# Performance work log

Hardware: AMD Instinct MI355X
Metric: run time of the kernel (lower is better)

## Reference

```python
import jax, jax.numpy as jnp
import numpy as np

B, S, H = 2, 2048, 4096
NH, NKV, HD = 32, 8, 128
N_REP = NH // NKV
SCALING = HD ** -0.5


def rotate_half(x):
    x1, x2 = x[..., : HD // 2], x[..., HD // 2 :]
    return jnp.concatenate((-x2, x1), axis=-1)


def setup_inputs() -> dict:
    key = jax.random.key(0)
    ks = jax.random.split(key, 8)
    hidden_states = jax.random.normal(ks[0], (B, S, H), dtype=jnp.float32)
    # RoPE tables computed as in Llama (deterministic, realistic values)
    inv_freq = 1.0 / (10000.0 ** (jnp.arange(0, HD, 2, dtype=jnp.float32) / HD))
    t = jnp.arange(S, dtype=jnp.float32)
    freqs = jnp.einsum('s,d->sd', t, inv_freq)
    emb = jnp.concatenate((freqs, freqs), axis=-1)  # [S, HD]
    cos = jnp.broadcast_to(jnp.cos(emb)[None], (B, S, HD))
    sin = jnp.broadcast_to(jnp.sin(emb)[None], (B, S, HD))
    # additive causal mask [B,1,S,S]
    causal = jnp.where(jnp.tril(jnp.ones((S, S), dtype=bool)), 0.0, -1e9).astype(jnp.float32)
    attention_mask = jnp.broadcast_to(causal[None, None], (B, 1, S, S))
    std = 0.02
    Wq = jax.random.normal(ks[1], (NH * HD, H), dtype=jnp.float32) * std
    Wk = jax.random.normal(ks[2], (NKV * HD, H), dtype=jnp.float32) * std
    Wv = jax.random.normal(ks[3], (NKV * HD, H), dtype=jnp.float32) * std
    Wo = jax.random.normal(ks[4], (H, NH * HD), dtype=jnp.float32) * std
    return dict(hidden_states=hidden_states, cos=cos, sin=sin,
                attention_mask=attention_mask, Wq=Wq, Wk=Wk, Wv=Wv, Wo=Wo)


def reference(hidden_states, cos, sin, attention_mask, Wq, Wk, Wv, Wo):
    b, s, _ = hidden_states.shape
    # projections (torch Linear: x @ W.T), split into heads -> [B, nH, S, HD]
    q = (hidden_states @ Wq.T).reshape(b, s, NH, HD).transpose(0, 2, 1, 3)
    k = (hidden_states @ Wk.T).reshape(b, s, NKV, HD).transpose(0, 2, 1, 3)
    v = (hidden_states @ Wv.T).reshape(b, s, NKV, HD).transpose(0, 2, 1, 3)
    # RoPE: cos/sin [B,S,HD] -> [B,1,S,HD]
    c, sn = cos[:, None], sin[:, None]
    q = q * c + rotate_half(q) * sn
    k = k * c + rotate_half(k) * sn
    # GQA: repeat kv heads
    k = jnp.repeat(k, N_REP, axis=1)
    v = jnp.repeat(v, N_REP, axis=1)
    scores = jnp.einsum('bhqd,bhkd->bhqk', q, k) * SCALING + attention_mask
    attn = jax.nn.softmax(scores.astype(jnp.float32), axis=-1).astype(q.dtype)
    out = jnp.einsum('bhqk,bhkd->bhqd', attn, v)
    out = out.transpose(0, 2, 1, 3).reshape(b, s, NH * HD)
    return out @ Wo.T
```

## Files before the change

kernel.cpp:

```cpp
#include <hip/hip_runtime.h>
#include <stdint.h>

typedef unsigned short u16;
typedef __attribute__((ext_vector_type(8))) short short8;
typedef __attribute__((ext_vector_type(4))) float f32x4;
typedef __attribute__((ext_vector_type(16))) float f32x16;
typedef __attribute__((ext_vector_type(4))) u16 u16x4;

static constexpr float SCALE = 0.08838834764831845f;
static constexpr float QSCALE = 0.12752459769642898f;

__device__ __forceinline__ u16 f2bf(float f) {
    union { float f; unsigned u; } x; x.f = f;
    unsigned r = x.u + 0x7fffu + ((x.u >> 16) & 1u);
    return (u16)(r >> 16);
}
__device__ __forceinline__ float bf2f(u16 b) {
    union { unsigned u; float f; } x; x.u = ((unsigned)b) << 16;
    return x.f;
}
__device__ __forceinline__ unsigned cvt_pk_bf16(float lo, float hi_) {
    unsigned r;
    asm("v_cvt_pk_bf16_f32 %0, %1, %2" : "=v"(r) : "v"(lo), "v"(hi_));
    return r;
}

__global__ __launch_bounds__(256) void convert5_kernel(const float* __restrict__ s0, const float* __restrict__ s1,
                                                       const float* __restrict__ s2, const float* __restrict__ s3,
                                                       const float* __restrict__ s4,
                                                       u16* __restrict__ d0, u16* __restrict__ d1,
                                                       u16* __restrict__ d2, u16* __restrict__ d3,
                                                       u16* __restrict__ d4) {
    const int V0 = 4194304, V1 = 8388608, V2 = 9437184, V3 = 10485760, V4 = 14680064;
    const int stride = gridDim.x * blockDim.x;
    for (int i = blockIdx.x * blockDim.x + threadIdx.x; i < V4; i += stride) {
        const float* sp; u16* dp; int off;
        if (i < V0)      { sp = s0; dp = d0; off = i; }
        else if (i < V1) { sp = s1; dp = d1; off = i - V0; }
        else if (i < V2) { sp = s2; dp = d2; off = i - V1; }
        else if (i < V3) { sp = s3; dp = d3; off = i - V2; }
        else             { sp = s4; dp = d4; off = i - V3; }
        float4 v = *reinterpret_cast<const float4*>(sp + (size_t)off * 4);
        u16x4 o;
        o.x = f2bf(v.x); o.y = f2bf(v.y); o.z = f2bf(v.z); o.w = f2bf(v.w);
        *reinterpret_cast<u16x4*>(dp + (size_t)off * 4) = o;
    }
}

template<int OUT_MODE>
__global__ __launch_bounds__(256) void gemm_bt(const u16* __restrict__ A,
                                               const u16* __restrict__ B,
                                               void* __restrict__ Cv,
                                               int M, int N, int K) {
    constexpr int BK = 64;
    __shared__ u16 sA[128 * BK];
    __shared__ u16 sB[128 * BK];
    const int tid = threadIdx.x;
    const int wid = tid >> 6, lane = tid & 63;
    const int lrow = lane & 15, lgrp = lane >> 4;
    const int row0 = blockIdx.x * 128, col0 = blockIdx.y * 128;
    const int wr = (wid >> 1) * 64, wc = (wid & 1) * 64;

    f32x4 acc[4][4] = {};

    const int NT = K / BK;
    for (int kt = 0; kt < NT; ++kt) {
        const int k0 = kt * BK;
        __syncthreads();
        #pragma unroll
        for (int rnd = 0; rnd < 4; ++rnd) {
            const int eoff = (rnd * 256 + tid) * 8;
            const int r = eoff >> 6, c = eoff & 63;
            const int gc = c ^ ((r & 7) << 3);
            const int ldsoff = rnd * 2048 + wid * 512;
            __builtin_amdgcn_global_load_lds(
                (const __attribute__((address_space(1))) void*)(A + (size_t)(row0 + r) * K + k0 + gc),
                (__attribute__((address_space(3))) void*)(&sA[ldsoff]), 16, 0, 0);
            __builtin_amdgcn_global_load_lds(
                (const __attribute__((address_space(1))) void*)(B + (size_t)(col0 + r) * K + k0 + gc),
                (__attribute__((address_space(3))) void*)(&sB[ldsoff]), 16, 0, 0);
        }
        __syncthreads();
        #pragma unroll
        for (int kk = 0; kk < 2; ++kk) {
            const int koff = kk * 32 + lgrp * 8;
            short8 af[4], bfr[4];
            #pragma unroll
            for (int m = 0; m < 4; ++m) {
                const int rr = wr + m * 16 + lrow;
                af[m] = *(const short8*)&sA[rr * BK + (koff ^ ((rr & 7) << 3))];
            }
            #pragma unroll
            for (int n = 0; n < 4; ++n) {
                const int rr = wc + n * 16 + lrow;
                bfr[n] = *(const short8*)&sB[rr * BK + (koff ^ ((rr & 7) << 3))];
            }
            #pragma unroll
            for (int m = 0; m < 4; ++m)
                #pragma unroll
                for (int n = 0; n < 4; ++n)
                    acc[m][n] = __builtin_amdgcn_mfma_f32_16x16x32_bf16(af[m], bfr[n], acc[m][n], 0, 0, 0);
        }
    }

    const int orow = row0 + wr + lgrp * 4;
    const int ocol = col0 + wc + lrow;
    if (OUT_MODE == 0) {
        u16* C = (u16*)Cv;
        #pragma unroll
        for (int m = 0; m < 4; ++m)
            #pragma unroll
            for (int n = 0; n < 4; ++n)
                #pragma unroll
                for (int r = 0; r < 4; ++r)
                    C[(size_t)(orow + m * 16 + r) * N + ocol + n * 16] = f2bf(acc[m][n][r]);
    } else {
        u16* C = (u16*)Cv;
        #pragma unroll
        for (int m = 0; m < 4; ++m)
            #pragma unroll
            for (int n = 0; n < 4; ++n) {
                u16x4 pk;
                pk.x = f2bf(acc[m][n][0]); pk.y = f2bf(acc[m][n][1]);
                pk.z = f2bf(acc[m][n][2]); pk.w = f2bf(acc[m][n][3]);
                *(u16x4*)&C[(size_t)(ocol + n * 16) * M + orow + m * 16] = pk;
            }
    }
}

template<int OUT_MODE>
__global__ __launch_bounds__(512, 2) void gemm256v2(const u16* __restrict__ A,
                                                    const u16* __restrict__ B,
                                                    void* __restrict__ Cv,
                                                    int M, int N, int K) {
    __shared__ u16 sA[2][2][256 * 32];
    __shared__ u16 sB[2][2][256 * 32];
    const int tid = threadIdx.x;
    const int wid = tid >> 6, lane = tid & 63;
    const int lrow = lane & 15, lgrp = lane >> 4;

    const int nbn = N >> 8;
    const int total = (M >> 8) * nbn;
    int bid = blockIdx.x;
    if ((total & 7) == 0) { const int cpx = total >> 3; bid = (bid & 7) * cpx + (bid >> 3); }
    const int row0 = (bid / nbn) * 256, col0 = (bid % nbn) * 256;
    const int wr = (wid >> 2) * 128, wc = (wid & 3) * 64;

    f32x4 acc[8][4] = {};

    const int rS0 = wid * 32 + (lane >> 2);
    const int uS = lane & 3;

    auto stageA = [&](int nb, int kt, int kkh) {
        const int k0 = kt * 64 + kkh * 32;
        #pragma unroll
        for (int g = 0; g < 2; ++g) {
            const int r = rS0 + g * 16;
            const int cs = k0 + ((uS ^ ((r >> 1) & 3)) << 3);
            __builtin_amdgcn_global_load_lds(
                (const __attribute__((address_space(1))) void*)(A + (size_t)(row0 + r) * K + cs),
                (__attribute__((address_space(3))) void*)(&sA[nb][kkh][(wid * 32 + g * 16) * 32]), 16, 0, 0);
        }
    };
    auto stageB = [&](int nb, int kt, int kkh) {
        const int k0 = kt * 64 + kkh * 32;
        #pragma unroll
        for (int g = 0; g < 2; ++g) {
            const int r = rS0 + g * 16;
            const int cs = k0 + ((uS ^ ((r >> 1) & 3)) << 3);
            __builtin_amdgcn_global_load_lds(
                (const __attribute__((address_space(1))) void*)(B + (size_t)(col0 + r) * K + cs),
                (__attribute__((address_space(3))) void*)(&sB[nb][kkh][(wid * 32 + g * 16) * 32]), 16, 0, 0);
        }
    };

    auto rdA = [&](int buf, int kkh, int fr) -> short8 {
        const int r = wr + fr * 16 + lrow;
        return *(const short8*)&sA[buf][kkh][r * 32 + ((lgrp ^ ((r >> 1) & 3)) << 3)];
    };
    auto rdB = [&](int buf, int kkh, int fc) -> short8 {
        const int r = wc + fc * 16 + lrow;
        return *(const short8*)&sB[buf][kkh][r * 32 + ((lgrp ^ ((r >> 1) & 3)) << 3)];
    };

    const int NK = K >> 6;
    stageA(0, 0, 0); stageB(0, 0, 0); stageA(0, 0, 1); stageB(0, 0, 1);
    asm volatile("s_waitcnt vmcnt(4)" ::: "memory");
    __builtin_amdgcn_s_barrier();

    for (int kt = 0; kt < NK; ++kt) {
        const int buf = kt & 1, nb = buf ^ 1;
        const bool st = (kt + 1 < NK);
        short8 a[4], b[4], a2[4];

        #pragma unroll
        for (int fr = 0; fr < 4; ++fr) a[fr] = rdA(buf, 0, fr);
        #pragma unroll
        for (int fc = 0; fc < 4; ++fc) b[fc] = rdB(buf, 0, fc);
        if (st) stageA(nb, kt + 1, 0);
        __builtin_amdgcn_sched_barrier(0);
        __builtin_amdgcn_s_barrier();
        asm volatile("s_waitcnt lgkmcnt(0)" ::: "memory");
        __builtin_amdgcn_sched_barrier(0);
        __builtin_amdgcn_s_setprio(1);
        #pragma unroll
        for (int fr = 0; fr < 4; ++fr)
            #pragma unroll
            for (int fc = 0; fc < 4; ++fc)
                acc[fr][fc] = __builtin_amdgcn_mfma_f32_16x16x32_bf16(a[fr], b[fc], acc[fr][fc], 0, 0, 0);
        __builtin_amdgcn_s_setprio(0);
        __builtin_amdgcn_sched_barrier(0);
        __builtin_amdgcn_s_barrier();

        #pragma unroll
        for (int fr = 0; fr < 4; ++fr) a2[fr] = rdA(buf, 0, fr + 4);
        if (st) stageB(nb, kt + 1, 0);
        __builtin_amdgcn_sched_barrier(0);
        __builtin_amdgcn_s_barrier();
        asm volatile("s_waitcnt lgkmcnt(0)" ::: "memory");
        __builtin_amdgcn_sched_barrier(0);
        __builtin_amdgcn_s_setprio(1);
        #pragma unroll
        for (int fr = 0; fr < 4; ++fr)
            #pragma unroll
            for (int fc = 0; fc < 4; ++fc)
                acc[fr + 4][fc] = __builtin_amdgcn_mfma_f32_16x16x32_bf16(a2[fr], b[fc], acc[fr + 4][fc], 0, 0, 0);
        __builtin_amdgcn_s_setprio(0);
        __builtin_amdgcn_sched_barrier(0);
        if (st) { asm volatile("s_waitcnt vmcnt(4)" ::: "memory"); }
        else    { asm volatile("s_waitcnt vmcnt(0)" ::: "memory"); }
        __builtin_amdgcn_s_barrier();

        #pragma unroll
        for (int fr = 0; fr < 4; ++fr) a[fr] = rdA(buf, 1, fr);
        #pragma unroll
        for (int fc = 0; fc < 4; ++fc) b[fc] = rdB(buf, 1, fc);
        if (st) stageA(nb, kt + 1, 1);
        __builtin_amdgcn_sched_barrier(0);
        __builtin_amdgcn_s_barrier();
        asm volatile("s_waitcnt lgkmcnt(0)" ::: "memory");
        __builtin_amdgcn_sched_barrier(0);
        __builtin_amdgcn_s_setprio(1);
        #pragma unroll
        for (int fr = 0; fr < 4; ++fr)
            #pragma unroll
            for (int fc = 0; fc < 4; ++fc)
                acc[fr][fc] = __builtin_amdgcn_mfma_f32_16x16x32_bf16(a[fr], b[fc], acc[fr][fc], 0, 0, 0);
        __builtin_amdgcn_s_setprio(0);
        __builtin_amdgcn_sched_barrier(0);
        __builtin_amdgcn_s_barrier();

        #pragma unroll
        for (int fr = 0; fr < 4; ++fr) a2[fr] = rdA(buf, 1, fr + 4);
        if (st) stageB(nb, kt + 1, 1);
        __builtin_amdgcn_sched_barrier(0);
        __builtin_amdgcn_s_barrier();
        asm volatile("s_waitcnt lgkmcnt(0)" ::: "memory");
        __builtin_amdgcn_sched_barrier(0);
        __builtin_amdgcn_s_setprio(1);
        #pragma unroll
        for (int fr = 0; fr < 4; ++fr)
            #pragma unroll
            for (int fc = 0; fc < 4; ++fc)
                acc[fr + 4][fc] = __builtin_amdgcn_mfma_f32_16x16x32_bf16(a2[fr], b[fc], acc[fr + 4][fc], 0, 0, 0);
        __builtin_amdgcn_s_setprio(0);
        __builtin_amdgcn_sched_barrier(0);
        if (st) { asm volatile("s_waitcnt vmcnt(4)" ::: "memory"); }
        __builtin_amdgcn_s_barrier();
    }

    const int orow = row0 + wr + lgrp * 4;
    const int ocol = col0 + wc + lrow;
    if (OUT_MODE == 2) {
        float* C = (float*)Cv;
        #pragma unroll
        for (int m = 0; m < 8; ++m)
            #pragma unroll
            for (int n = 0; n < 4; ++n)
                #pragma unroll
                for (int r = 0; r < 4; ++r)
                    C[(size_t)(orow + m * 16 + r) * N + ocol + n * 16] = acc[m][n][r];
    } else {
        u16* C = (u16*)Cv;
        #pragma unroll
        for (int m = 0; m < 8; ++m)
            #pragma unroll
            for (int n = 0; n < 4; ++n)
                #pragma unroll
                for (int r = 0; r < 4; ++r)
                    C[(size_t)(orow + m * 16 + r) * N + ocol + n * 16] = f2bf(acc[m][n][r]);
    }
}

template<int NHEADS>
__global__ __launch_bounds__(256) void rope_kernel(u16* __restrict__ X,
                                                   const float* __restrict__ cosb,
                                                   const float* __restrict__ sinb,
                                                   float scale) {
    constexpr int LH = (NHEADS == 32) ? 5 : 3;
    const int total = 2 * 2048 * NHEADS * 64;
    const int stride = gridDim.x * blockDim.x;
    for (int i = blockIdx.x * blockDim.x + threadIdx.x; i < total; i += stride) {
        const int d = i & 63;
        const int h = (i >> 6) & (NHEADS - 1);
        const int rs = i >> (6 + LH);
        const size_t base = (size_t)rs * (NHEADS * 128) + h * 128 + d;
        const float c = cosb[rs * 128 + d] * scale;
        const float sn = sinb[rs * 128 + d] * scale;
        const float x1 = bf2f(X[base]);
        const float x2 = bf2f(X[base + 64]);
        X[base] = f2bf(x1 * c - x2 * sn);
        X[base + 64] = f2bf(x2 * c + x1 * sn);
    }
}

__global__ __launch_bounds__(512, 2) void attn_kernel(const u16* __restrict__ Q,
                                                      const u16* __restrict__ K,
                                                      const u16* __restrict__ Vt,
                                                      u16* __restrict__ AO) {
    __shared__ u16 sK[2][64 * 128];
    __shared__ u16 sV[2][128 * 64];
    const int tid = threadIdx.x;
    const int wid = tid >> 6, lane = tid & 63;
    const int l31 = lane & 31, hi = lane >> 5;

    const int gg = blockIdx.x >> 6;
    const int bx = (gg < 4) ? gg : 11 - gg;
    const int rem = blockIdx.x & 63;
    const int h = rem >> 1;
    const int b = rem & 1;
    const int hkv = h >> 2;
    const int rs0 = b * 2048;
    const int q0 = bx * 256;
    const int qw = q0 + wid * 32;
    const int q_lane = qw + l31;

    short8 qf[8];
    {
        const u16* qb = Q + (size_t)(rs0 + q_lane) * 4096 + h * 128 + hi * 8;
        #pragma unroll
        for (int f = 0; f < 8; ++f) qf[f] = *(const short8*)(qb + f * 16);
    }

    f32x16 accO[4] = {};
    float m_c = -1e30f, l_c = 0.f;

    auto stage = [&](int bf, int t) {
        const int kv0 = t * 64;
        #pragma unroll
        for (int rnd = 0; rnd < 2; ++rnd) {
            {
                const int e = rnd * 4096 + tid * 8;
                const int r = e >> 7, c = e & 127;
                const int cs = c ^ ((r & 15) << 3);
                __builtin_amdgcn_global_load_lds(
                    (const __attribute__((address_space(1))) void*)(K + (size_t)(rs0 + kv0 + r) * 1024 + hkv * 128 + cs),
                    (__attribute__((address_space(3))) void*)(&sK[bf][rnd * 4096 + wid * 512]), 16, 0, 0);
            }
            {
                const int e = rnd * 4096 + tid * 8;
                const int r = e >> 6, c = e & 63;
                const int cs = c ^ ((r & 7) << 3);
                __builtin_amdgcn_global_load_lds(
                    (const __attribute__((address_space(1))) void*)(Vt + (size_t)(hkv * 128 + r) * 4096 + rs0 + kv0 + cs),
                    (__attribute__((address_space(3))) void*)(&sV[bf][rnd * 4096 + wid * 512]), 16, 0, 0);
            }
        }
    };

    const int NT = 4 * (bx + 1);
    stage(0, 0);
    __syncthreads();
    int buf = 0;

    for (int t = 0; t < NT; ++t) {
        if (t + 1 < NT) stage(buf ^ 1, t + 1);
        const int kv0 = t * 64;

        if (kv0 <= qw + 31) {
            f32x16 sc[2] = {};
            #pragma unroll
            for (int f = 0; f < 8; ++f) {
                const int col = f * 16 + hi * 8;
                const int r0 = l31, r1 = 32 + l31;
                short8 k0 = *(const short8*)&sK[buf][r0 * 128 + (col ^ ((r0 & 15) << 3))];
                short8 k1 = *(const short8*)&sK[buf][r1 * 128 + (col ^ ((r1 & 15) << 3))];
                sc[0] = __builtin_amdgcn_mfma_f32_32x32x16_bf16(k0, qf[f], sc[0], 0, 0, 0);
                sc[1] = __builtin_amdgcn_mfma_f32_32x32x16_bf16(k1, qf[f], sc[1], 0, 0, 0);
            }

            if (kv0 + 63 > q_lane) {
                #pragma unroll
                for (int blk = 0; blk < 2; ++blk)
                    #pragma unroll
                    for (int r = 0; r < 16; ++r) {
                        const int kv_abs = kv0 + blk * 32 + ((r & 3) + 8 * (r >> 2) + 4 * hi);
                        if (kv_abs > q_lane) sc[blk][r] = -1e30f;
                    }
            }

            float mx = sc[0][0];
            #pragma unroll
            for (int blk = 0; blk < 2; ++blk)
                #pragma unroll
                for (int r = 0; r < 16; ++r) mx = fmaxf(mx, sc[blk][r]);
            mx = fmaxf(mx, __shfl_xor(mx, 32));

            if (!__all(mx <= m_c + 8.0f)) {
                const float sclf = __builtin_amdgcn_exp2f(m_c - mx);
                m_c = mx;
                l_c *= sclf;
                float sclq[16];
                #pragma unroll
                for (int r = 0; r < 16; ++r)
                    sclq[r] = __shfl(sclf, (r & 3) + 8 * (r >> 2) + 4 * hi);
                #pragma unroll
                for (int d4 = 0; d4 < 4; ++d4)
                    #pragma unroll
                    for (int r = 0; r < 16; ++r) accO[d4][r] *= sclq[r];
            }
            float ssum = 0.f;
            #pragma unroll
            for (int blk = 0; blk < 2; ++blk)
                #pragma unroll
                for (int r = 0; r < 16; ++r) {
                    const float p = __builtin_amdgcn_exp2f(sc[blk][r] - m_c);
                    sc[blk][r] = p;
                    ssum += p;
                }
            ssum += __shfl_xor(ssum, 32);
            l_c += ssum;

            #pragma unroll
            for (int blk = 0; blk < 2; ++blk) {
                #pragma unroll
                for (int tt = 0; tt < 2; ++tt) {
                    const unsigned cv00 = cvt_pk_bf16(sc[blk][8 * tt + 0], sc[blk][8 * tt + 1]);
                    const unsigned cv01 = cvt_pk_bf16(sc[blk][8 * tt + 2], sc[blk][8 * tt + 3]);
                    const unsigned cv10 = cvt_pk_bf16(sc[blk][8 * tt + 4], sc[blk][8 * tt + 5]);
                    const unsigned cv11 = cvt_pk_bf16(sc[blk][8 * tt + 6], sc[blk][8 * tt + 7]);
                    const unsigned s00 = __shfl_xor(cv00, 32);
                    const unsigned s01 = __shfl_xor(cv01, 32);
                    const unsigned s10 = __shfl_xor(cv10, 32);
                    const unsigned s11 = __shfl_xor(cv11, 32);
                    union { unsigned w[4]; short8 v; } pa;
                    pa.w[0] = hi ? s10 : cv00;
                    pa.w[1] = hi ? s11 : cv01;
                    pa.w[2] = hi ? cv10 : s00;
                    pa.w[3] = hi ? cv11 : s01;
                    const int kvb = blk * 32 + tt * 16 + hi * 8;
                    #pragma unroll
                    for (int d4 = 0; d4 < 4; ++d4) {
                        const int vr = d4 * 32 + l31;
                        short8 vf = *(const short8*)&sV[buf][vr * 64 + (kvb ^ ((vr & 7) << 3))];
                        accO[d4] = __builtin_amdgcn_mfma_f32_32x32x16_bf16(pa.v, vf, accO[d4], 0, 0, 0);
                    }
                }
            }
        }
        __syncthreads();
        buf ^= 1;
    }

    const float invl = 1.0f / l_c;
    float invq[16];
    #pragma unroll
    for (int r = 0; r < 16; ++r)
        invq[r] = __shfl(invl, (r & 3) + 8 * (r >> 2) + 4 * hi);
    #pragma unroll
    for (int d4 = 0; d4 < 4; ++d4)
        #pragma unroll
        for (int r = 0; r < 16; ++r) {
            const int q = qw + (r & 3) + 8 * (r >> 2) + 4 * hi;
            AO[(size_t)(rs0 + q) * 4096 + h * 128 + d4 * 32 + l31] = f2bf(accO[d4][r] * invq[r]);
        }
}

extern "C" void kernel_launch(void* const* d_in, const int* in_sizes, int n_in,
                              void* d_out, int out_size, void* d_ws, size_t ws_size,
                              hipStream_t stream) {
    const float* hs   = (const float*)d_in[0];
    const float* cosp = (const float*)d_in[1];
    const float* sinp = (const float*)d_in[2];
    const float* Wq = (const float*)d_in[4];
    const float* Wk = (const float*)d_in[5];
    const float* Wv = (const float*)d_in[6];
    const float* Wo = (const float*)d_in[7];

    u16* Xb = (u16*)d_out;
    u16* Qb = (u16*)d_out + 16777216;
    char* w = (char*)d_ws;
    u16* Wqb = (u16*)w; w += 33554432;
    u16* Wkb = (u16*)w; w += 8388608;
    u16* Wvb = (u16*)w; w += 8388608;
    u16* Wob = (u16*)w; w += 33554432;
    u16* Kb  = (u16*)w; w += 8388608;
    u16* Vtb = (u16*)w; w += 8388608;
    u16* AOb = (u16*)w; w += 33554432;

    convert5_kernel<<<4096, 256, 0, stream>>>(hs, Wq, Wk, Wv, Wo, Xb, Wqb, Wkb, Wvb, Wob);

    gemm256v2<0><<<256, 512, 0, stream>>>(Xb, Wqb, Qb, 4096, 4096, 4096);
    gemm_bt<0><<<dim3(32, 8), 256, 0, stream>>>(Xb, Wkb, Kb, 4096, 1024, 4096);
    gemm_bt<1><<<dim3(32, 8), 256, 0, stream>>>(Xb, Wvb, Vtb, 4096, 1024, 4096);

    rope_kernel<32><<<2048, 256, 0, stream>>>(Qb, cosp, sinp, QSCALE);
    rope_kernel<8><<<1024, 256, 0, stream>>>(Kb, cosp, sinp, 1.0f);

    attn_kernel<<<512, 512, 0, stream>>>(Qb, Kb, Vtb, AOb);

    gemm256v2<2><<<256, 512, 0, stream>>>(AOb, Wob, (float*)d_out, 4096, 4096, 4096);
}
```

Measured before the change: 599.9 us.

## Drop intra-iteration barriers in big GEMM, merge K/V GEMMs and RoPE launches

```diff
diff --git a/kernel.cpp b/kernel.cpp
--- a/kernel.cpp
+++ b/kernel.cpp
@@ -47,18 +47,24 @@
     }
 }
 
-template<int OUT_MODE>
-__global__ __launch_bounds__(256) void gemm_bt(const u16* __restrict__ A,
-                                               const u16* __restrict__ B,
-                                               void* __restrict__ Cv,
-                                               int M, int N, int K) {
-    constexpr int BK = 64;
+__global__ __launch_bounds__(256) void gemm_kv(const u16* __restrict__ A,
+                                               const u16* __restrict__ Bk,
+                                               const u16* __restrict__ Bv,
+                                               u16* __restrict__ Ck,
+                                               u16* __restrict__ Cvt) {
+    constexpr int K = 4096, N = 1024, BK = 64;
     __shared__ u16 sA[128 * BK];
     __shared__ u16 sB[128 * BK];
     const int tid = threadIdx.x;
     const int wid = tid >> 6, lane = tid & 63;
     const int lrow = lane & 15, lgrp = lane >> 4;
-    const int row0 = blockIdx.x * 128, col0 = blockIdx.y * 128;
+
+    int bid = blockIdx.x;
+    { const int cpx = 512 >> 3; bid = (bid & 7) * cpx + (bid >> 3); }
+    const bool isV = bid >= 256;
+    const int b2 = bid & 255;
+    const int row0 = (b2 >> 3) * 128, col0 = (b2 & 7) * 128;
+    const u16* __restrict__ B = isV ? Bv : Bk;
     const int wr = (wid >> 1) * 64, wc = (wid & 1) * 64;
 
     f32x4 acc[4][4] = {};
@@ -105,17 +111,15 @@
 
     const int orow = row0 + wr + lgrp * 4;
     const int ocol = col0 + wc + lrow;
-    if (OUT_MODE == 0) {
-        u16* C = (u16*)Cv;
+    if (!isV) {
         #pragma unroll
         for (int m = 0; m < 4; ++m)
             #pragma unroll
             for (int n = 0; n < 4; ++n)
                 #pragma unroll
                 for (int r = 0; r < 4; ++r)
-                    C[(size_t)(orow + m * 16 + r) * N + ocol + n * 16] = f2bf(acc[m][n][r]);
+                    Ck[(size_t)(orow + m * 16 + r) * N + ocol + n * 16] = f2bf(acc[m][n][r]);
     } else {
-        u16* C = (u16*)Cv;
         #pragma unroll
         for (int m = 0; m < 4; ++m)
             #pragma unroll
@@ -123,13 +127,13 @@
                 u16x4 pk;
                 pk.x = f2bf(acc[m][n][0]); pk.y = f2bf(acc[m][n][1]);
                 pk.z = f2bf(acc[m][n][2]); pk.w = f2bf(acc[m][n][3]);
-                *(u16x4*)&C[(size_t)(ocol + n * 16) * M + orow + m * 16] = pk;
+                *(u16x4*)&Cvt[(size_t)(ocol + n * 16) * 4096 + orow + m * 16] = pk;
             }
     }
 }
 
 template<int OUT_MODE>
-__global__ __launch_bounds__(512, 2) void gemm256v2(const u16* __restrict__ A,
+__global__ __launch_bounds__(512, 2) void gemm256v3(const u16* __restrict__ A,
                                                     const u16* __restrict__ B,
                                                     void* __restrict__ Cv,
                                                     int M, int N, int K) {
@@ -187,6 +191,7 @@
     stageA(0, 0, 0); stageB(0, 0, 0); stageA(0, 0, 1); stageB(0, 0, 1);
     asm volatile("s_waitcnt vmcnt(4)" ::: "memory");
     __builtin_amdgcn_s_barrier();
+    __builtin_amdgcn_sched_barrier(0);
 
     for (int kt = 0; kt < NK; ++kt) {
         const int buf = kt & 1, nb = buf ^ 1;
@@ -198,8 +203,6 @@
         #pragma unroll
         for (int fc = 0; fc < 4; ++fc) b[fc] = rdB(buf, 0, fc);
         if (st) stageA(nb, kt + 1, 0);
-        __builtin_amdgcn_sched_barrier(0);
-        __builtin_amdgcn_s_barrier();
         asm volatile("s_waitcnt lgkmcnt(0)" ::: "memory");
         __builtin_amdgcn_sched_barrier(0);
         __builtin_amdgcn_s_setprio(1);
@@ -209,14 +212,10 @@
             for (int fc = 0; fc < 4; ++fc)
                 acc[fr][fc] = __builtin_amdgcn_mfma_f32_16x16x32_bf16(a[fr], b[fc], acc[fr][fc], 0, 0, 0);
         __builtin_amdgcn_s_setprio(0);
-        __builtin_amdgcn_sched_barrier(0);
-        __builtin_amdgcn_s_barrier();
 
         #pragma unroll
         for (int fr = 0; fr < 4; ++fr) a2[fr] = rdA(buf, 0, fr + 4);
         if (st) stageB(nb, kt + 1, 0);
-        __builtin_amdgcn_sched_barrier(0);
-        __builtin_amdgcn_s_barrier();
         asm volatile("s_waitcnt lgkmcnt(0)" ::: "memory");
         __builtin_amdgcn_sched_barrier(0);
         __builtin_amdgcn_s_setprio(1);
@@ -226,18 +225,16 @@
             for (int fc = 0; fc < 4; ++fc)
                 acc[fr + 4][fc] = __builtin_amdgcn_mfma_f32_16x16x32_bf16(a2[fr], b[fc], acc[fr + 4][fc], 0, 0, 0);
         __builtin_amdgcn_s_setprio(0);
-        __builtin_amdgcn_sched_barrier(0);
         if (st) { asm volatile("s_waitcnt vmcnt(4)" ::: "memory"); }
         else    { asm volatile("s_waitcnt vmcnt(0)" ::: "memory"); }
         __builtin_amdgcn_s_barrier();
+        __builtin_amdgcn_sched_barrier(0);
 
         #pragma unroll
         for (int fr = 0; fr < 4; ++fr) a[fr] = rdA(buf, 1, fr);
         #pragma unroll
         for (int fc = 0; fc < 4; ++fc) b[fc] = rdB(buf, 1, fc);
         if (st) stageA(nb, kt + 1, 1);
-        __builtin_amdgcn_sched_barrier(0);
-        __builtin_amdgcn_s_barrier();
         asm volatile("s_waitcnt lgkmcnt(0)" ::: "memory");
         __builtin_amdgcn_sched_barrier(0);
         __builtin_amdgcn_s_setprio(1);
@@ -247,14 +244,10 @@
             for (int fc = 0; fc < 4; ++fc)
                 acc[fr][fc] = __builtin_amdgcn_mfma_f32_16x16x32_bf16(a[fr], b[fc], acc[fr][fc], 0, 0, 0);
         __builtin_amdgcn_s_setprio(0);
-        __builtin_amdgcn_sched_barrier(0);
-        __builtin_amdgcn_s_barrier();
 
         #pragma unroll
         for (int fr = 0; fr < 4; ++fr) a2[fr] = rdA(buf, 1, fr + 4);
         if (st) stageB(nb, kt + 1, 1);
-        __builtin_amdgcn_sched_barrier(0);
-        __builtin_amdgcn_s_barrier();
         asm volatile("s_waitcnt lgkmcnt(0)" ::: "memory");
         __builtin_amdgcn_sched_barrier(0);
         __builtin_amdgcn_s_setprio(1);
@@ -264,9 +257,9 @@
             for (int fc = 0; fc < 4; ++fc)
                 acc[fr + 4][fc] = __builtin_amdgcn_mfma_f32_16x16x32_bf16(a2[fr], b[fc], acc[fr + 4][fc], 0, 0, 0);
         __builtin_amdgcn_s_setprio(0);
-        __builtin_amdgcn_sched_barrier(0);
         if (st) { asm volatile("s_waitcnt vmcnt(4)" ::: "memory"); }
         __builtin_amdgcn_s_barrier();
+        __builtin_amdgcn_sched_barrier(0);
     }
 
     const int orow = row0 + wr + lgrp * 4;
@@ -292,19 +285,20 @@
     }
 }
 
-template<int NHEADS>
-__global__ __launch_bounds__(256) void rope_kernel(u16* __restrict__ X,
-                                                   const float* __restrict__ cosb,
-                                                   const float* __restrict__ sinb,
-                                                   float scale) {
-    constexpr int LH = (NHEADS == 32) ? 5 : 3;
-    const int total = 2 * 2048 * NHEADS * 64;
+__global__ __launch_bounds__(256) void rope_fused(u16* __restrict__ Q, u16* __restrict__ Kk,
+                                                  const float* __restrict__ cosb,
+                                                  const float* __restrict__ sinb) {
+    const int totQ = 2 * 2048 * 32 * 64;
+    const int total = totQ + 2 * 2048 * 8 * 64;
     const int stride = gridDim.x * blockDim.x;
     for (int i = blockIdx.x * blockDim.x + threadIdx.x; i < total; i += stride) {
-        const int d = i & 63;
-        const int h = (i >> 6) & (NHEADS - 1);
-        const int rs = i >> (6 + LH);
-        const size_t base = (size_t)rs * (NHEADS * 128) + h * 128 + d;
+        u16* X; int idx, nhm, sh; float scale;
+        if (i < totQ) { X = Q; idx = i; nhm = 31; sh = 11; scale = QSCALE; }
+        else          { X = Kk; idx = i - totQ; nhm = 7; sh = 9; scale = 1.0f; }
+        const int d = idx & 63;
+        const int h = (idx >> 6) & nhm;
+        const int rs = idx >> sh;
+        const size_t base = (size_t)rs * ((nhm + 1) * 128) + h * 128 + d;
         const float c = cosb[rs * 128 + d] * scale;
         const float sn = sinb[rs * 128 + d] * scale;
         const float x1 = bf2f(X[base]);
@@ -500,14 +494,12 @@
 
     convert5_kernel<<<4096, 256, 0, stream>>>(hs, Wq, Wk, Wv, Wo, Xb, Wqb, Wkb, Wvb, Wob);
 
-    gemm256v2<0><<<256, 512, 0, stream>>>(Xb, Wqb, Qb, 4096, 4096, 4096);
-    gemm_bt<0><<<dim3(32, 8), 256, 0, stream>>>(Xb, Wkb, Kb, 4096, 1024, 4096);
-    gemm_bt<1><<<dim3(32, 8), 256, 0, stream>>>(Xb, Wvb, Vtb, 4096, 1024, 4096);
-
-    rope_kernel<32><<<2048, 256, 0, stream>>>(Qb, cosp, sinp, QSCALE);
-    rope_kernel<8><<<1024, 256, 0, stream>>>(Kb, cosp, sinp, 1.0f);
+    gemm256v3<0><<<256, 512, 0, stream>>>(Xb, Wqb, Qb, 4096, 4096, 4096);
+    gemm_kv<<<512, 256, 0, stream>>>(Xb, Wkb, Wvb, Kb, Vtb);
+
+    rope_fused<<<2048, 256, 0, stream>>>(Qb, Kb, cosp, sinp);
 
     attn_kernel<<<512, 512, 0, stream>>>(Qb, Kb, Vtb, AOb);
 
-    gemm256v2<2><<<256, 512, 0, stream>>>(AOb, Wob, (float*)d_out, 4096, 4096, 4096);
-}
+    gemm256v3<2><<<256, 512, 0, stream>>>(AOb, Wob, (float*)d_out, 4096, 4096, 4096);
+}
```

New measurement: 526.4 us. 1.14x faster.
